# Kernel tuning notes

Measured on AMD Instinct MI355X. Metric: run time of the kernel, lower is better.

## Reference

```python
import jax, jax.numpy as jnp
import numpy as np

GROUPS = 32
EPS = 1e-5


def setup_inputs() -> dict:
    key = jax.random.key(0)
    ks = jax.random.split(key, 7)
    B, C, H, W = 16, 512, 32, 32
    return {
        "x": jax.random.normal(ks[0], (B, C, H, W), jnp.float32),
        "norm_w": jax.random.uniform(ks[1], (C,), jnp.float32, 0.5, 1.5),
        "norm_b": jax.random.normal(ks[2], (C,), jnp.float32) * 0.1,
        "qkv_w": jax.random.normal(ks[3], (3 * C, C), jnp.float32) * (C ** -0.5),
        "qkv_b": jax.random.normal(ks[4], (3 * C,), jnp.float32) * 0.01,
        "proj_w": jax.random.normal(ks[5], (C, C), jnp.float32) * (C ** -0.5),
        "proj_b": jax.random.normal(ks[6], (C,), jnp.float32) * 0.01,
        "num_heads": 8,
    }


def _group_norm(x, w, b):
    # x: (B, C, T); GroupNorm over (C//G, T) per group, per-channel affine
    B, C, T = x.shape
    xg = x.reshape(B, GROUPS, C // GROUPS, T)
    mean = jnp.mean(xg, axis=(2, 3), keepdims=True)
    var = jnp.var(xg, axis=(2, 3), keepdims=True)
    xn = ((xg - mean) * jax.lax.rsqrt(var + EPS)).reshape(B, C, T)
    return xn * w[None, :, None] + b[None, :, None]


def reference(x, norm_w, norm_b, qkv_w, qkv_b, proj_w, proj_b, num_heads):
    B, C, H, W = x.shape
    T = H * W
    xf = x.reshape(B, C, T)
    # qkv conv1x1: (B, 3C, T)
    qkv = jnp.einsum('oc,bct->bot', qkv_w, _group_norm(xf, norm_w, norm_b)) \
        + qkv_b[None, :, None]
    # split heads: (B*H, 3*hd, T) then chunk on channel dim
    BH = B * num_heads
    qkv = qkv.reshape(BH, 3 * C // num_heads, T)
    q, k, v = jnp.split(qkv, 3, axis=1)  # each (BH, hd, T)
    hd = C // num_heads
    scale = hd ** -0.25
    # scores (BH, T, T), softmax in fp32 then cast back (matches torch)
    scores = jnp.einsum('bct,bcs->bts', q * scale, k * scale)
    w = jax.nn.softmax(scores.astype(jnp.float32), axis=-1).astype(scores.dtype)
    h = jnp.einsum('bts,bcs->bct', w, v)  # (BH, hd, T)
    h = h.reshape(B, C, T)
    h = jnp.einsum('oc,bct->bot', proj_w, h) + proj_b[None, :, None]
    return (h + xf).reshape(B, C, H, W)
```

## Files before the change

### kernel.cpp

```cpp
#include <hip/hip_runtime.h>

typedef unsigned short u16;
typedef unsigned int u32;
typedef __bf16 bf16x8 __attribute__((ext_vector_type(8)));
typedef float f32x4 __attribute__((ext_vector_type(4)));
typedef float f32x16 __attribute__((ext_vector_type(16)));

#define SCALE_QK 0.35355339059327373f
#define LOG2E 1.4426950408889634f

__device__ __forceinline__ u16 f2bf(float f) {
  u32 u = __float_as_uint(f);
  u += 0x7FFFu + ((u >> 16) & 1u);
  return (u16)(u >> 16);
}

__device__ __forceinline__ void gload16(const u16* g, u16* l) {
  __builtin_amdgcn_global_load_lds((const __attribute__((address_space(1))) void*)g,
                                   (__attribute__((address_space(3))) void*)l, 16, 0, 0);
}

__device__ __forceinline__ int rswz(int r) { return (r & 7) ^ ((r >> 3) & 3); }

__global__ __launch_bounds__(256) void k_convert(const float* __restrict__ src,
                                                 u16* __restrict__ dst, int n4) {
  int i = blockIdx.x * 256 + threadIdx.x;
  if (i >= n4) return;
  float4 v = ((const float4*)src)[i];
  u32 lo = (u32)f2bf(v.x) | ((u32)f2bf(v.y) << 16);
  u32 hi = (u32)f2bf(v.z) | ((u32)f2bf(v.w) << 16);
  ((uint2*)dst)[i] = make_uint2(lo, hi);
}

__global__ __launch_bounds__(256) void k_groupnorm(const float* __restrict__ x,
                                                   const float* __restrict__ nw,
                                                   const float* __restrict__ nb,
                                                   u16* __restrict__ gnt) {
  const int b = blockIdx.x >> 5;
  const int g = blockIdx.x & 31;
  const int tid = threadIdx.x;
  const float* xg = x + ((size_t)b * 512 + g * 16) * 1024;

  float s = 0.f, ss = 0.f;
#pragma unroll
  for (int it = 0; it < 16; ++it) {
    float4 v = ((const float4*)xg)[tid + it * 256];
    s += v.x + v.y + v.z + v.w;
    ss += v.x * v.x + v.y * v.y + v.z * v.z + v.w * v.w;
  }
#pragma unroll
  for (int off = 32; off >= 1; off >>= 1) {
    s += __shfl_xor(s, off);
    ss += __shfl_xor(ss, off);
  }
  __shared__ float red[8];
  const int wid = tid >> 6, lane = tid & 63;
  if (lane == 0) { red[wid] = s; red[4 + wid] = ss; }
  __syncthreads();
  const float mean = (red[0] + red[1] + red[2] + red[3]) * (1.f / 16384.f);
  const float ex2 = (red[4] + red[5] + red[6] + red[7]) * (1.f / 16384.f);
  const float rstd = rsqrtf(ex2 - mean * mean + 1e-5f);

  const int ci = tid & 15, tt = tid >> 4;
  const int c = g * 16 + ci;
  const float wc = nw[c] * rstd;
  const float bc = nb[c] - mean * wc;
  const float* xc = xg + (size_t)ci * 1024;
  u16* dst = gnt + (size_t)b * 1024 * 512 + c;
#pragma unroll 8
  for (int t = tt; t < 1024; t += 16) {
    dst[(size_t)t * 512] = f2bf(xc[t] * wc + bc);
  }
}

template <int MODE>
__global__ __launch_bounds__(512) void k_gemm(const u16* __restrict__ A,
                                              const u16* __restrict__ Bw,
                                              const float* __restrict__ bias,
                                              u16* __restrict__ Qb, u16* __restrict__ Kb,
                                              u16* __restrict__ Vb,
                                              const float* __restrict__ xres,
                                              float* __restrict__ out) {
  __shared__ u16 As[2][128][64];
  __shared__ u16 Bs[2][128][64];
  const int tid = threadIdx.x;
  const int lane = tid & 63, wid = tid >> 6;
  const int wr = wid >> 1, wc = wid & 1;
  const int fid = blockIdx.x;
  const int m0 = (fid & 127) * 128;
  const int n0 = (fid >> 7) * 128;
  const int l15 = lane & 15, l4 = lane >> 4;
  const f32x4 fzero = {0.f, 0.f, 0.f, 0.f};

  f32x4 acc[2][4];
#pragma unroll
  for (int i = 0; i < 2; ++i)
#pragma unroll
    for (int j = 0; j < 4; ++j) acc[i][j] = fzero;

  const int lrow = (tid & 63) >> 3;
  const int lchunk = tid & 7;

  auto stage = [&](int bi, int kt) {
#pragma unroll
    for (int rd = 0; rd < 2; ++rd) {
      const int rbase = wid * 8 + rd * 64;
      const int r = rbase + lrow;
      const int q = lchunk ^ (r & 7);
      gload16(A + ((size_t)(m0 + r) * 512 + kt * 64 + q * 8), &As[bi][rbase][0]);
      gload16(Bw + ((size_t)(n0 + r) * 512 + kt * 64 + q * 8), &Bs[bi][rbase][0]);
    }
  };

  stage(0, 0);
  stage(1, 1);

  for (int kt = 0; kt < 8; ++kt) {
    if (kt < 7) {
      asm volatile("s_waitcnt vmcnt(4)" ::: "memory");
    } else {
      asm volatile("s_waitcnt vmcnt(0)" ::: "memory");
    }
    __builtin_amdgcn_s_barrier();
    const int buf = kt & 1;
#pragma unroll
    for (int ks = 0; ks < 2; ++ks) {
      bf16x8 af[2], bfr[4];
#pragma unroll
      for (int mi = 0; mi < 2; ++mi) {
        const int row = wr * 32 + mi * 16 + l15;
        af[mi] = *(const bf16x8*)&As[buf][row][(((ks << 2) + l4) ^ (row & 7)) << 3];
      }
#pragma unroll
      for (int ni = 0; ni < 4; ++ni) {
        const int row = wc * 64 + ni * 16 + l15;
        bfr[ni] = *(const bf16x8*)&Bs[buf][row][(((ks << 2) + l4) ^ (row & 7)) << 3];
      }
#pragma unroll
      for (int mi = 0; mi < 2; ++mi)
#pragma unroll
        for (int ni = 0; ni < 4; ++ni)
          acc[mi][ni] = __builtin_amdgcn_mfma_f32_16x16x32_bf16(af[mi], bfr[ni], acc[mi][ni], 0, 0, 0);
    }
    asm volatile("s_waitcnt lgkmcnt(0)" ::: "memory");
    __builtin_amdgcn_sched_barrier(0);
    __builtin_amdgcn_s_barrier();
    if (kt < 6) stage(buf, kt + 2);
  }

#pragma unroll
  for (int ni = 0; ni < 4; ++ni) {
    const int o = n0 + wc * 64 + ni * 16 + l15;
    const float bo = bias[o];
    if (MODE == 0) {
      const int h = o / 192;
      const int jo = o - h * 192;
      const int typ = jo >> 6;
      const int ci = jo & 63;
#pragma unroll
      for (int mi = 0; mi < 2; ++mi) {
        const int mrow = m0 + wr * 32 + mi * 16 + l4 * 4;
        const int b = mrow >> 10, t0 = mrow & 1023;
#pragma unroll
        for (int jj = 0; jj < 4; ++jj) {
          const float v = acc[mi][ni][jj] + bo;
          const int t = t0 + jj;
          if (typ == 0)
            Qb[(((size_t)(b * 8 + h) * 1024 + t) << 6) + ci] = f2bf(v * (SCALE_QK * LOG2E));
          else if (typ == 1)
            Kb[(((size_t)(b * 8 + h) * 1024 + t) << 6) + ci] = f2bf(v * SCALE_QK);
          else
            Vb[(((size_t)(b * 8 + h) * 64 + ci) << 10) + t] = f2bf(v);
        }
      }
    } else {
#pragma unroll
      for (int mi = 0; mi < 2; ++mi) {
        const int mrow = m0 + wr * 32 + mi * 16 + l4 * 4;
        const int b = mrow >> 10, t0 = mrow & 1023;
        const size_t base = ((size_t)b * 512 + o) * 1024 + t0;
        const float4 xr = *(const float4*)(xres + base);
        float4 ov;
        ov.x = acc[mi][ni][0] + bo + xr.x;
        ov.y = acc[mi][ni][1] + bo + xr.y;
        ov.z = acc[mi][ni][2] + bo + xr.z;
        ov.w = acc[mi][ni][3] + bo + xr.w;
        *(float4*)(out + base) = ov;
      }
    }
  }
}

__global__ __launch_bounds__(128) void k_attn(const u16* __restrict__ Qb,
                                              const u16* __restrict__ Kb,
                                              const u16* __restrict__ Vb,
                                              u16* __restrict__ ht) {
  __shared__ u16 Ks[2][64][64];
  __shared__ u16 Vs[2][64][64];
  const int tid = threadIdx.x;
  const int lane = tid & 63, wid = tid >> 6;
  const int l31 = lane & 31, hi = lane >> 5;
  const int fid = blockIdx.x;
  const int bh = fid & 127, qt = fid >> 7;
  const int b = bh >> 3, head = bh & 7;
  const int lrow = lane >> 3, lchunk = lane & 7;
  const int rsw = rswz(l31);

  bf16x8 qf0[4], qf1[4];
  {
    const u16* qp0 = Qb + (((size_t)bh * 1024 + qt * 128 + wid * 64 + l31) << 6) + hi * 8;
    const u16* qp1 = qp0 + (32 << 6);
#pragma unroll
    for (int kc = 0; kc < 4; ++kc) {
      qf0[kc] = *(const bf16x8*)(qp0 + kc * 16);
      qf1[kc] = *(const bf16x8*)(qp1 + kc * 16);
    }
  }

  bf16x8 onesf;
#pragma unroll
  for (int i = 0; i < 8; ++i) onesf[i] = (l31 == 0) ? (__bf16)1.0f : (__bf16)0.0f;

  f32x16 oacc[2][2], osum[2];
#pragma unroll
  for (int g = 0; g < 2; ++g)
#pragma unroll
    for (int r = 0; r < 16; ++r) { oacc[g][0][r] = 0.f; oacc[g][1][r] = 0.f; osum[g][r] = 0.f; }

  auto stageKV = [&](int bi, int st) {
    const int s0 = st * 64;
#pragma unroll
    for (int rd = 0; rd < 4; ++rd) {
      const int rbase = wid * 32 + rd * 8;
      const int r = rbase + lrow;
      const int q = lchunk ^ rswz(r);
      gload16(Kb + (((size_t)bh * 1024 + s0 + r) << 6) + q * 8, &Ks[bi][rbase][0]);
      gload16(Vb + (((size_t)bh * 64 + r) << 10) + s0 + q * 8, &Vs[bi][rbase][0]);
    }
  };

  stageKV(0, 0);
  stageKV(1, 1);

  for (int st = 0; st < 16; ++st) {
    if (st < 15) {
      asm volatile("s_waitcnt vmcnt(8)" ::: "memory");
    } else {
      asm volatile("s_waitcnt vmcnt(0)" ::: "memory");
    }
    __builtin_amdgcn_s_barrier();
    const int buf = st & 1;

#pragma unroll
    for (int cb = 0; cb < 2; ++cb) {
      f32x16 sacc0, sacc1;
#pragma unroll
      for (int r = 0; r < 16; ++r) { sacc0[r] = 0.f; sacc1[r] = 0.f; }
      __builtin_amdgcn_s_setprio(1);
#pragma unroll
      for (int kc = 0; kc < 4; ++kc) {
        const int r = cb * 32 + l31;
        const bf16x8 kb = *(const bf16x8*)&Ks[buf][r][((((kc << 1) | hi)) ^ rsw) << 3];
        sacc0 = __builtin_amdgcn_mfma_f32_32x32x16_bf16(kb, qf0[kc], sacc0, 0, 0, 0);
        sacc1 = __builtin_amdgcn_mfma_f32_32x32x16_bf16(kb, qf1[kc], sacc1, 0, 0, 0);
      }
      __builtin_amdgcn_s_setprio(0);
      float p0[16], p1[16];
#pragma unroll
      for (int r = 0; r < 16; ++r) {
        asm("v_exp_f32 %0, %1" : "=v"(p0[r]) : "v"(sacc0[r]));
        asm("v_exp_f32 %0, %1" : "=v"(p1[r]) : "v"(sacc1[r]));
      }

#pragma unroll
      for (int ksl = 0; ksl < 2; ++ksl) {
        u32 A0, A1, B0, B1, C0, C1, D0, D1;
        asm("v_cvt_pk_bf16_f32 %0, %1, %2" : "=v"(A0) : "v"(p0[8 * ksl + 0]), "v"(p0[8 * ksl + 1]));
        asm("v_cvt_pk_bf16_f32 %0, %1, %2" : "=v"(A1) : "v"(p0[8 * ksl + 2]), "v"(p0[8 * ksl + 3]));
        asm("v_cvt_pk_bf16_f32 %0, %1, %2" : "=v"(B0) : "v"(p0[8 * ksl + 4]), "v"(p0[8 * ksl + 5]));
        asm("v_cvt_pk_bf16_f32 %0, %1, %2" : "=v"(B1) : "v"(p0[8 * ksl + 6]), "v"(p0[8 * ksl + 7]));
        asm volatile("v_permlane32_swap_b32 %0, %1" : "+v"(A0), "+v"(B0));
        asm volatile("v_permlane32_swap_b32 %0, %1" : "+v"(A1), "+v"(B1));
        asm("v_cvt_pk_bf16_f32 %0, %1, %2" : "=v"(C0) : "v"(p1[8 * ksl + 0]), "v"(p1[8 * ksl + 1]));
        asm("v_cvt_pk_bf16_f32 %0, %1, %2" : "=v"(C1) : "v"(p1[8 * ksl + 2]), "v"(p1[8 * ksl + 3]));
        asm("v_cvt_pk_bf16_f32 %0, %1, %2" : "=v"(D0) : "v"(p1[8 * ksl + 4]), "v"(p1[8 * ksl + 5]));
        asm("v_cvt_pk_bf16_f32 %0, %1, %2" : "=v"(D1) : "v"(p1[8 * ksl + 6]), "v"(p1[8 * ksl + 7]));
        asm volatile("v_permlane32_swap_b32 %0, %1" : "+v"(C0), "+v"(D0));
        asm volatile("v_permlane32_swap_b32 %0, %1" : "+v"(C1), "+v"(D1));
        union { u32 w[4]; bf16x8 v; } pa0, pa1;
        pa0.w[0] = A0; pa0.w[1] = A1; pa0.w[2] = B0; pa0.w[3] = B1;
        pa1.w[0] = C0; pa1.w[1] = C1; pa1.w[2] = D0; pa1.w[3] = D1;
        const int ks = cb * 2 + ksl;
        __builtin_amdgcn_s_setprio(1);
#pragma unroll
        for (int db = 0; db < 2; ++db) {
          const int r = db * 32 + l31;
          const bf16x8 vb = *(const bf16x8*)&Vs[buf][r][((((ks << 1) | hi)) ^ rsw) << 3];
          oacc[0][db] = __builtin_amdgcn_mfma_f32_32x32x16_bf16(pa0.v, vb, oacc[0][db], 0, 0, 0);
          oacc[1][db] = __builtin_amdgcn_mfma_f32_32x32x16_bf16(pa1.v, vb, oacc[1][db], 0, 0, 0);
        }
        osum[0] = __builtin_amdgcn_mfma_f32_32x32x16_bf16(pa0.v, onesf, osum[0], 0, 0, 0);
        osum[1] = __builtin_amdgcn_mfma_f32_32x32x16_bf16(pa1.v, onesf, osum[1], 0, 0, 0);
        __builtin_amdgcn_s_setprio(0);
      }
    }

    asm volatile("s_waitcnt lgkmcnt(0)" ::: "memory");
    __builtin_amdgcn_sched_barrier(0);
    __builtin_amdgcn_s_barrier();
    if (st < 14) stageKV(buf, st + 2);
  }

#pragma unroll
  for (int g = 0; g < 2; ++g) {
    float inv[16];
#pragma unroll
    for (int r = 0; r < 16; ++r) {
      const float ls = __shfl(osum[g][r], lane & 32);
      inv[r] = 1.f / ls;
    }
    const int tg = qt * 128 + wid * 64 + g * 32;
#pragma unroll
    for (int db = 0; db < 2; ++db) {
#pragma unroll
      for (int r = 0; r < 16; ++r) {
        const int t = tg + (r & 3) + 8 * (r >> 2) + 4 * hi;
        const int cg = head * 64 + db * 32 + l31;
        ht[((size_t)b * 1024 + t) * 512 + cg] = f2bf(oacc[g][db][r] * inv[r]);
      }
    }
  }
}

extern "C" void kernel_launch(void* const* d_in, const int* in_sizes, int n_in,
                              void* d_out, int out_size, void* d_ws, size_t ws_size,
                              hipStream_t stream) {
  const float* x = (const float*)d_in[0];
  const float* norm_w = (const float*)d_in[1];
  const float* norm_b = (const float*)d_in[2];
  const float* qkv_w = (const float*)d_in[3];
  const float* qkv_b = (const float*)d_in[4];
  const float* proj_w = (const float*)d_in[5];
  const float* proj_b = (const float*)d_in[6];
  float* out = (float*)d_out;

  char* ws = (char*)d_ws;
  u16* qkvw = (u16*)(ws + 0);
  u16* projw = (u16*)(ws + 1572864);
  u16* gnt = (u16*)(ws + 2097152);
  u16* Qb = (u16*)(ws + 18874368);
  u16* Kb = (u16*)(ws + 35651584);
  u16* Vb = (u16*)(ws + 52428800);
  u16* ht = (u16*)(ws + 69206016);

  k_convert<<<768, 256, 0, stream>>>(qkv_w, qkvw, 196608);
  k_convert<<<256, 256, 0, stream>>>(proj_w, projw, 65536);
  k_groupnorm<<<512, 256, 0, stream>>>(x, norm_w, norm_b, gnt);
  k_gemm<0><<<1536, 512, 0, stream>>>(gnt, qkvw, qkv_b, Qb, Kb, Vb, nullptr, nullptr);
  k_attn<<<1024, 128, 0, stream>>>(Qb, Kb, Vb, ht);
  k_gemm<1><<<512, 512, 0, stream>>>(ht, projw, proj_b, nullptr, nullptr, nullptr, x, out);
}
```

Before: 166.2 us.

## Fuse prep kernels and triple-buffer attention KV with 4-wave blocks

Merges the two weight-conversion kernels and groupnorm into one launch, dispatching on block index. The attention kernel moves to 256-thread blocks covering 256 queries, so each KV tile is shared by four waves. It also uses a three-deep LDS ring that issues the next load right after the barrier, which drops the second barrier per step. This aims to cut launch overhead, halve KV global traffic per query and overlap loads with compute, at the cost of more LDS per block and possibly lower occupancy.

```diff
diff --git a/kernel.cpp b/kernel.cpp
--- a/kernel.cpp
+++ b/kernel.cpp
@@ -22,23 +22,30 @@
 
 __device__ __forceinline__ int rswz(int r) { return (r & 7) ^ ((r >> 3) & 3); }
 
-__global__ __launch_bounds__(256) void k_convert(const float* __restrict__ src,
-                                                 u16* __restrict__ dst, int n4) {
-  int i = blockIdx.x * 256 + threadIdx.x;
-  if (i >= n4) return;
-  float4 v = ((const float4*)src)[i];
-  u32 lo = (u32)f2bf(v.x) | ((u32)f2bf(v.y) << 16);
-  u32 hi = (u32)f2bf(v.z) | ((u32)f2bf(v.w) << 16);
-  ((uint2*)dst)[i] = make_uint2(lo, hi);
-}
-
-__global__ __launch_bounds__(256) void k_groupnorm(const float* __restrict__ x,
-                                                   const float* __restrict__ nw,
-                                                   const float* __restrict__ nb,
-                                                   u16* __restrict__ gnt) {
-  const int b = blockIdx.x >> 5;
-  const int g = blockIdx.x & 31;
+__global__ __launch_bounds__(256) void k_prep(const float* __restrict__ x,
+                                              const float* __restrict__ nw,
+                                              const float* __restrict__ nb,
+                                              const float* __restrict__ qkvw_f,
+                                              const float* __restrict__ projw_f,
+                                              u16* __restrict__ gnt,
+                                              u16* __restrict__ qkvw,
+                                              u16* __restrict__ projw) {
+  const int bid = blockIdx.x;
   const int tid = threadIdx.x;
+
+  if (bid >= 512) {
+    const float* src = (bid < 1280) ? qkvw_f : projw_f;
+    u16* dst = (bid < 1280) ? qkvw : projw;
+    const int i = (bid - ((bid < 1280) ? 512 : 1280)) * 256 + tid;
+    float4 v = ((const float4*)src)[i];
+    u32 lo = (u32)f2bf(v.x) | ((u32)f2bf(v.y) << 16);
+    u32 hi = (u32)f2bf(v.z) | ((u32)f2bf(v.w) << 16);
+    ((uint2*)dst)[i] = make_uint2(lo, hi);
+    return;
+  }
+
+  const int b = bid >> 5;
+  const int g = bid & 31;
   const float* xg = x + ((size_t)b * 512 + g * 16) * 1024;
 
   float s = 0.f, ss = 0.f;
@@ -191,12 +198,12 @@
   }
 }
 
-__global__ __launch_bounds__(128) void k_attn(const u16* __restrict__ Qb,
+__global__ __launch_bounds__(256) void k_attn(const u16* __restrict__ Qb,
                                               const u16* __restrict__ Kb,
                                               const u16* __restrict__ Vb,
                                               u16* __restrict__ ht) {
-  __shared__ u16 Ks[2][64][64];
-  __shared__ u16 Vs[2][64][64];
+  __shared__ u16 Ks[3][64][64];
+  __shared__ u16 Vs[3][64][64];
   const int tid = threadIdx.x;
   const int lane = tid & 63, wid = tid >> 6;
   const int l31 = lane & 31, hi = lane >> 5;
@@ -208,7 +215,7 @@
 
   bf16x8 qf0[4], qf1[4];
   {
-    const u16* qp0 = Qb + (((size_t)bh * 1024 + qt * 128 + wid * 64 + l31) << 6) + hi * 8;
+    const u16* qp0 = Qb + (((size_t)bh * 1024 + qt * 256 + wid * 64 + l31) << 6) + hi * 8;
     const u16* qp1 = qp0 + (32 << 6);
 #pragma unroll
     for (int kc = 0; kc < 4; ++kc) {
@@ -230,8 +237,8 @@
   auto stageKV = [&](int bi, int st) {
     const int s0 = st * 64;
 #pragma unroll
-    for (int rd = 0; rd < 4; ++rd) {
-      const int rbase = wid * 32 + rd * 8;
+    for (int rd = 0; rd < 2; ++rd) {
+      const int rbase = wid * 8 + rd * 32;
       const int r = rbase + lrow;
       const int q = lchunk ^ rswz(r);
       gload16(Kb + (((size_t)bh * 1024 + s0 + r) << 6) + q * 8, &Ks[bi][rbase][0]);
@@ -242,14 +249,15 @@
   stageKV(0, 0);
   stageKV(1, 1);
 
+  int bufc = 0, bufs = 2;
   for (int st = 0; st < 16; ++st) {
     if (st < 15) {
-      asm volatile("s_waitcnt vmcnt(8)" ::: "memory");
+      asm volatile("s_waitcnt vmcnt(4)" ::: "memory");
     } else {
       asm volatile("s_waitcnt vmcnt(0)" ::: "memory");
     }
     __builtin_amdgcn_s_barrier();
-    const int buf = st & 1;
+    if (st < 14) stageKV(bufs, st + 2);
 
 #pragma unroll
     for (int cb = 0; cb < 2; ++cb) {
@@ -260,7 +268,7 @@
 #pragma unroll
       for (int kc = 0; kc < 4; ++kc) {
         const int r = cb * 32 + l31;
-        const bf16x8 kb = *(const bf16x8*)&Ks[buf][r][((((kc << 1) | hi)) ^ rsw) << 3];
+        const bf16x8 kb = *(const bf16x8*)&Ks[bufc][r][((((kc << 1) | hi)) ^ rsw) << 3];
         sacc0 = __builtin_amdgcn_mfma_f32_32x32x16_bf16(kb, qf0[kc], sacc0, 0, 0, 0);
         sacc1 = __builtin_amdgcn_mfma_f32_32x32x16_bf16(kb, qf1[kc], sacc1, 0, 0, 0);
       }
@@ -295,7 +303,7 @@
 #pragma unroll
         for (int db = 0; db < 2; ++db) {
           const int r = db * 32 + l31;
-          const bf16x8 vb = *(const bf16x8*)&Vs[buf][r][((((ks << 1) | hi)) ^ rsw) << 3];
+          const bf16x8 vb = *(const bf16x8*)&Vs[bufc][r][((((ks << 1) | hi)) ^ rsw) << 3];
           oacc[0][db] = __builtin_amdgcn_mfma_f32_32x32x16_bf16(pa0.v, vb, oacc[0][db], 0, 0, 0);
           oacc[1][db] = __builtin_amdgcn_mfma_f32_32x32x16_bf16(pa1.v, vb, oacc[1][db], 0, 0, 0);
         }
@@ -305,10 +313,8 @@
       }
     }
 
-    asm volatile("s_waitcnt lgkmcnt(0)" ::: "memory");
-    __builtin_amdgcn_sched_barrier(0);
-    __builtin_amdgcn_s_barrier();
-    if (st < 14) stageKV(buf, st + 2);
+    bufc = (bufc == 2) ? 0 : bufc + 1;
+    bufs = (bufs == 2) ? 0 : bufs + 1;
   }
 
 #pragma unroll
@@ -319,7 +325,7 @@
       const float ls = __shfl(osum[g][r], lane & 32);
       inv[r] = 1.f / ls;
     }
-    const int tg = qt * 128 + wid * 64 + g * 32;
+    const int tg = qt * 256 + wid * 64 + g * 32;
 #pragma unroll
     for (int db = 0; db < 2; ++db) {
 #pragma unroll
@@ -353,10 +359,8 @@
   u16* Vb = (u16*)(ws + 52428800);
   u16* ht = (u16*)(ws + 69206016);
 
-  k_convert<<<768, 256, 0, stream>>>(qkv_w, qkvw, 196608);
-  k_convert<<<256, 256, 0, stream>>>(proj_w, projw, 65536);
-  k_groupnorm<<<512, 256, 0, stream>>>(x, norm_w, norm_b, gnt);
+  k_prep<<<1536, 256, 0, stream>>>(x, norm_w, norm_b, qkv_w, proj_w, gnt, qkvw, projw);
   k_gemm<0><<<1536, 512, 0, stream>>>(gnt, qkvw, qkv_b, Qb, Kb, Vb, nullptr, nullptr);
-  k_attn<<<1024, 128, 0, stream>>>(Qb, Kb, Vb, ht);
+  k_attn<<<512, 256, 0, stream>>>(Qb, Kb, Vb, ht);
   k_gemm<1><<<512, 512, 0, stream>>>(ht, projw, proj_b, nullptr, nullptr, nullptr, x, out);
 }
```

Result: faster. 144.2 us (-13.3%).
